# Kernel tuning notes

Hardware: AMD Instinct MI355X
Metric: run time of the kernel (lower is better)

The kernel has to match this reference:

```python
import jax, jax.numpy as jnp
import numpy as np

D = 1024; H = 16; HD = 64; DEPTH = 8; INTERVAL = 4; CTX = 9; NUM_REG = 4
SOFTCAP = 50.0; EPS = 1e-6; ROPE_BASE = 10000.0; IN_DIM = 768; ADIM = 8; FREQ = 256; DH = 4096
B = 1; T = 16; LTOK = 256; S = LTOK + 2 + NUM_REG  # 262 tokens per frame


def setup_inputs() -> dict:
    key = jax.random.key(0)
    ks = jax.random.split(key, 24)
    s = 0.02
    n = jax.random.normal
    inp = {
        'noisy_latents': n(ks[0], (B, T, LTOK, IN_DIM), jnp.float32),
        'signal_levels': jax.random.uniform(ks[1], (B, T), jnp.float32),
        'actions': n(ks[2], (B, T, ADIM), jnp.float32),
        'input_proj_w': n(ks[3], (D, IN_DIM)) * s,
        'noise_w1': n(ks[4], (D, FREQ)) * s,
        'noise_b1': jnp.zeros((D,)),
        'noise_w2': n(ks[5], (D, D)) * s,
        'noise_b2': jnp.zeros((D,)),
        'base_action_embed': n(ks[6], (D,)) * s,
        'action_proj_w': n(ks[7], (D, ADIM)) * (s * 0.1),
        'action_proj_b': jnp.zeros((D,)),
        'register_tokens': n(ks[8], (NUM_REG, D)) * s,
        'ln1_w': jnp.ones((DEPTH, D)),
        's_wqkv': n(ks[9], (DEPTH, 3 * D, D)) * s,
        's_wo': n(ks[10], (DEPTH, D, D)) * s,
        's_qg': jnp.ones((DEPTH, HD)),
        's_kg': jnp.ones((DEPTH, HD)),
        'lnt_w': jnp.ones((DEPTH, D)),
        't_wqkv': n(ks[11], (DEPTH, 3 * D, D)) * s,
        't_wo': n(ks[12], (DEPTH, D, D)) * s,
        't_qg': jnp.ones((DEPTH, HD)),
        't_kg': jnp.ones((DEPTH, HD)),
        'ln2_w': jnp.ones((DEPTH, D)),
        'mlp_w12': n(ks[13], (DEPTH, 2 * DH, D)) * s,
        'mlp_w3': n(ks[14], (DEPTH, D, DH)) * s,
        'final_norm_w': jnp.ones((D,)),
        'out_w': n(ks[15], (IN_DIM, D)) * s,
        'out_b': jnp.zeros((IN_DIM,)),
    }
    return inp


def rms(x, w, eps=EPS):
    return x * jax.lax.rsqrt(jnp.mean(x * x, axis=-1, keepdims=True) + eps) * w


def rope_cache(seq_len):
    inv = ROPE_BASE ** (-jnp.arange(0, HD, 2, dtype=jnp.float32) / HD)  # [HD/2]
    f = jnp.arange(seq_len, dtype=jnp.float32)[:, None] * inv  # [S, HD/2]
    return jnp.cos(f), jnp.sin(f)


def apply_rope(x, cos, sin):
    # x: [..., S, HD]; cos/sin: [S, HD/2]
    x1, x2 = jnp.split(x, 2, axis=-1)
    return jnp.concatenate([x1 * cos - x2 * sin, x1 * sin + x2 * cos], axis=-1)


def attention(xn, wqkv, wo, qg, kg, cos, sin, mask):
    # xn: [B, G, S, D]; mask broadcastable to [..., S, S]
    lead = xn.shape[:-1]
    qkv = jnp.einsum('bgsd,ed->bgse', xn, wqkv)
    q, k, v = jnp.split(qkv, 3, axis=-1)
    def heads(z):
        return z.reshape(lead + (H, HD)).swapaxes(-2, -3)  # [B, G, H, S, HD]
    q, k, v = heads(q), heads(k), heads(v)
    q = rms(q, qg); k = rms(k, kg)  # qk-norm per head
    q = apply_rope(q, cos, sin); k = apply_rope(k, cos, sin)
    logits = jnp.einsum('bghqd,bghkd->bghqk', q, k) / np.sqrt(HD).astype(np.float32)
    logits = SOFTCAP * jnp.tanh(logits / SOFTCAP)  # attn logit softcapping
    logits = jnp.where(mask, logits, -1e30)
    p = jax.nn.softmax(logits, axis=-1)
    o = jnp.einsum('bghqk,bghkd->bghqd', p, v)
    o = o.swapaxes(-2, -3).reshape(lead + (H * HD,))
    return jnp.einsum('bgsd,ed->bgse', o, wo)


def timestep_embedding(t, dim=FREQ, max_period=10000.0):
    half = dim // 2
    freqs = jnp.exp(-np.log(max_period) * jnp.arange(half, dtype=jnp.float32) / half)
    args = t[:, None] * freqs
    return jnp.concatenate([jnp.cos(args), jnp.sin(args)], axis=-1)


def reference(noisy_latents, signal_levels, actions, input_proj_w, noise_w1, noise_b1,
              noise_w2, noise_b2, base_action_embed, action_proj_w, action_proj_b,
              register_tokens, ln1_w, s_wqkv, s_wo, s_qg, s_kg, lnt_w, t_wqkv, t_wo,
              t_qg, t_kg, ln2_w, mlp_w12, mlp_w3, final_norm_w, out_w, out_b):
    b, t, ltok, _ = noisy_latents.shape
    noisy_tokens = jnp.einsum('btld,ed->btle', noisy_latents, input_proj_w)  # [B,T,L,D]
    # timestep embedder (sinusoidal + MLP)
    emb = timestep_embedding(signal_levels.reshape(-1))
    sig = jax.nn.silu(emb @ noise_w1.T + noise_b1) @ noise_w2.T + noise_b2
    sig = sig.reshape(b, t, 1, D)
    act = base_action_embed + actions @ action_proj_w.T + action_proj_b  # [B,T,D]
    act = act[:, :, None, :]
    reg = jnp.broadcast_to(register_tokens, (b, t, NUM_REG, D))
    x = jnp.concatenate([sig, act, reg, noisy_tokens], axis=2)  # [B,T,S,D]
    s = x.shape[2]
    # spatial mask: full attention except frozen token (row 0) attends only to itself
    sm = jnp.ones((s, s), bool)
    sm = sm.at[0].set(False).at[0, 0].set(True)
    # temporal mask: causal with context window CTX
    ti = jnp.arange(t)
    tm = (ti[None, :] <= ti[:, None]) & (ti[None, :] >= ti[:, None] - CTX)
    s_cos, s_sin = rope_cache(s)
    t_cos, t_sin = rope_cache(t)
    for l in range(DEPTH):
        h = rms(x, ln1_w[l])
        x = x + attention(h, s_wqkv[l], s_wo[l], s_qg[l], s_kg[l], s_cos, s_sin, sm)
        if l % INTERVAL == 0:
            xt = x.swapaxes(1, 2)  # [B,S,T,D]
            h = rms(xt, lnt_w[l])
            xt = xt + attention(h, t_wqkv[l], t_wo[l], t_qg[l], t_kg[l], t_cos, t_sin, tm)
            x = xt.swapaxes(1, 2)
        h = rms(x, ln2_w[l])
        g = jnp.einsum('btsd,ed->btse', h, mlp_w12[l])
        g1, g2 = jnp.split(g, 2, axis=-1)
        x = x + jnp.einsum('btse,de->btsd', jax.nn.silu(g1) * g2, mlp_w3[l])
    latents = rms(x[..., NUM_REG + 2:, :], final_norm_w)
    return latents @ out_w.T + out_b  # [B,T,L,IN_DIM]
```

## Files before the change

kernel.cpp:

```cpp
#include <hip/hip_runtime.h>
#include <hip/hip_bf16.h>
#include <math.h>

#define T_ 16
#define S_ 262
#define D_ 1024
#define H_ 16
#define HD_ 64
#define DH_ 4096
#define NTOK (T_*S_)
#define LTOK_ 256
#define INDIM_ 768

typedef __attribute__((ext_vector_type(4))) float f32x4;
typedef __attribute__((ext_vector_type(8))) short s16x8;
typedef __attribute__((ext_vector_type(4))) short s16x4;

__device__ __forceinline__ short f2bf(float f) {
  union { float f; unsigned u; } v; v.f = f;
  unsigned r = v.u + 0x7fffu + ((v.u >> 16) & 1u);
  return (short)(r >> 16);
}
__device__ __forceinline__ float bf2f(short h) {
  union { unsigned u; float f; } v; v.u = ((unsigned)(unsigned short)h) << 16;
  return v.f;
}
__device__ __forceinline__ float softcap(float x) {
  float z = __expf(x * (2.0f / 50.0f));
  return 50.0f * (z - 1.0f) / (z + 1.0f);
}
__device__ __forceinline__ void gload16(const void* g, void* l) {
  __builtin_amdgcn_global_load_lds((const __attribute__((address_space(1))) void*)g,
                                   (__attribute__((address_space(3))) void*)l, 16, 0, 0);
}

template<int SMALL, int RESID, int BIAS, int OUT, int WB, int PERM, int PREP, int ROWMAP>
__global__ __launch_bounds__(256)
void gemm2(const short* __restrict__ A, const void* __restrict__ Wv,
           const float* __restrict__ bias, void* __restrict__ Cv,
           int M, int N, int K,
           const float* __restrict__ qg, const float* __restrict__ kg,
           const float* __restrict__ ctab, const float* __restrict__ stab)
{
  constexpr int BM   = SMALL ? 64 : 128;
  constexpr int MI   = SMALL ? 2 : 4;
  constexpr int WR   = SMALL ? 32 : 64;
  constexpr int NSTG = SMALL ? 2 : 4;
  __shared__ __align__(16) short As[BM*64];
  __shared__ __align__(16) short Bs[BM*64];
  const int tid = threadIdx.x;
  const int m0 = blockIdx.y * BM, n0 = blockIdx.x * BM;
  const int lane = tid & 63, wid = tid >> 6;
  const int wr = (wid >> 1) * WR, wc = (wid & 1) * WR;
  const int lr = lane & 15, lk = (lane >> 4) * 8;
  const short* Wb = (const short*)Wv;
  const float* Wf = (const float*)Wv;

  const f32x4 fzero = {0.f, 0.f, 0.f, 0.f};
  f32x4 acc[MI][MI];
  #pragma unroll
  for (int i = 0; i < MI; ++i)
    #pragma unroll
    for (int j = 0; j < MI; ++j) acc[i][j] = fzero;

  for (int k0 = 0; k0 < K; k0 += 64) {
    #pragma unroll
    for (int i = 0; i < NSTG; ++i) {
      int row = wid*(NSTG*8) + i*8 + (lane >> 3);
      int gm = m0 + row; if (gm >= M) gm = M - 1;
      int gc = (((lane & 7) ^ (row & 7)) << 3);
      gload16(A + (size_t)gm*K + k0 + gc, &As[(wid*(NSTG*8) + i*8)*64]);
    }
    if (WB) {
      #pragma unroll
      for (int i = 0; i < NSTG; ++i) {
        int row = wid*(NSTG*8) + i*8 + (lane >> 3);
        int gc = (((lane & 7) ^ (row & 7)) << 3);
        gload16(Wb + (size_t)(n0 + row)*K + k0 + gc, &Bs[(wid*(NSTG*8) + i*8)*64]);
      }
    } else {
      #pragma unroll
      for (int i = 0; i < NSTG; ++i) {
        int slot = tid + 256*i;
        int row = slot >> 3, c8 = (slot & 7) << 3;
        int gr = n0 + row;
        if (PERM) { int c = gr >> 5, q = gr & 31; gr = (q < 16) ? c*16 + q : DH_ + c*16 + (q - 16); }
        const float* wp = Wf + (size_t)gr*K + k0 + c8;
        float4 w0 = *(const float4*)wp, w1 = *(const float4*)(wp + 4);
        s16x8 b;
        b[0]=f2bf(w0.x); b[1]=f2bf(w0.y); b[2]=f2bf(w0.z); b[3]=f2bf(w0.w);
        b[4]=f2bf(w1.x); b[5]=f2bf(w1.y); b[6]=f2bf(w1.z); b[7]=f2bf(w1.w);
        *(s16x8*)&Bs[row*64 + (c8 ^ ((row & 7) << 3))] = b;
      }
    }
    __syncthreads();
    #pragma unroll
    for (int kh = 0; kh < 2; ++kh) {
      const int col0 = kh*32 + lk;
      s16x8 af[MI], bfr[MI];
      #pragma unroll
      for (int mi = 0; mi < MI; ++mi) {
        int row = wr + mi*16 + lr;
        af[mi] = *(const s16x8*)&As[row*64 + (col0 ^ ((row & 7) << 3))];
      }
      #pragma unroll
      for (int ni = 0; ni < MI; ++ni) {
        int row = wc + ni*16 + lr;
        bfr[ni] = *(const s16x8*)&Bs[row*64 + (col0 ^ ((row & 7) << 3))];
      }
      #pragma unroll
      for (int mi = 0; mi < MI; ++mi)
        #pragma unroll
        for (int ni = 0; ni < MI; ++ni)
          acc[mi][ni] = __builtin_amdgcn_mfma_f32_16x16x32_bf16(af[mi], bfr[ni], acc[mi][ni], 0, 0, 0);
    }
    __syncthreads();
  }
  const int gg = (lane >> 4) * 4;
  if constexpr (OUT == 2) {
    #pragma unroll
    for (int mi = 0; mi < MI; ++mi)
      #pragma unroll
      for (int np = 0; np < MI/2; ++np) {
        const int ni = np*2;
        const int ocol = ((n0 + wc + ni*16) >> 5) * 16 + lr;
        #pragma unroll
        for (int r = 0; r < 4; ++r) {
          int row = m0 + wr + mi*16 + gg + r;
          if (row < M) {
            float g = acc[mi][ni][r], v = acc[mi][ni+1][r];
            float sl = g / (1.f + __expf(-g));
            ((short*)Cv)[(size_t)row * (N >> 1) + ocol] = f2bf(sl * v);
          }
        }
      }
  } else if constexpr (PREP != 0) {
    const int colsec = n0 + wc;
    const bool isv = (colsec >= 2048);
    const float* gp = (colsec < 1024) ? qg : kg;
    float gv[MI];
    if (!isv) {
      #pragma unroll
      for (int ni = 0; ni < MI; ++ni) gv[ni] = gp[ni*16 + lr];
    }
    #pragma unroll
    for (int mi = 0; mi < MI; ++mi) {
      #pragma unroll
      for (int r = 0; r < 4; ++r) {
        int row = m0 + wr + mi*16 + gg + r;
        int rowc = row < M ? row : M - 1;
        float vv[MI];
        #pragma unroll
        for (int ni = 0; ni < MI; ++ni) vv[ni] = acc[mi][ni][r];
        if (!isv) {
          float ss = vv[0]*vv[0] + vv[1]*vv[1] + vv[2]*vv[2] + vv[3]*vv[3];
          ss += __shfl_xor(ss, 1);
          ss += __shfl_xor(ss, 2);
          ss += __shfl_xor(ss, 4);
          ss += __shfl_xor(ss, 8);
          float sc = rsqrtf(ss * (1.f/64.f) + 1e-6f);
          int pos = (PREP == 1) ? (rowc % S_) : (rowc / S_);
          float c0 = ctab[pos*32 + lr],      s0 = stab[pos*32 + lr];
          float c1 = ctab[pos*32 + 16 + lr], s1 = stab[pos*32 + 16 + lr];
          float a0 = vv[0]*sc*gv[0], a1 = vv[1]*sc*gv[1];
          float a2 = vv[2]*sc*gv[2], a3 = vv[3]*sc*gv[3];
          vv[0] = a0*c0 - a2*s0;
          vv[1] = a1*c1 - a3*s1;
          vv[2] = a0*s0 + a2*c0;
          vv[3] = a1*s1 + a3*c1;
        }
        if (row < M) {
          #pragma unroll
          for (int ni = 0; ni < MI; ++ni)
            ((short*)Cv)[(size_t)row * N + n0 + wc + ni*16 + lr] = f2bf(vv[ni]);
        }
      }
    }
  } else {
    #pragma unroll
    for (int mi = 0; mi < MI; ++mi)
      #pragma unroll
      for (int ni = 0; ni < MI; ++ni) {
        int col = n0 + wc + ni*16 + lr;
        #pragma unroll
        for (int r = 0; r < 4; ++r) {
          int row = m0 + wr + mi*16 + gg + r;
          if (row < M) {
            float v = acc[mi][ni][r];
            if (BIAS) v += bias[col];
            size_t orow = ROWMAP ? (size_t)((row >> 8) * S_ + 6 + (row & 255)) : (size_t)row;
            size_t idx = orow * N + col;
            if (RESID == 1)       ((float*)Cv)[idx] += v;
            else if (OUT == 1)    ((short*)Cv)[idx]  = f2bf(v);
            else                  ((float*)Cv)[idx]  = v;
          }
        }
      }
  }
}

template<int FINAL>
__global__ __launch_bounds__(256)
void rmsnorm_k(const float* __restrict__ x, const float* __restrict__ w, short* __restrict__ h)
{
  const int lane = threadIdx.x & 63;
  const int row = blockIdx.x*4 + (threadIdx.x >> 6);
  const int xrow = FINAL ? ((row >> 8) * S_ + 6 + (row & 255)) : row;
  const float* xp = x + (size_t)xrow*D_;
  float4 v[4];
  #pragma unroll
  for (int j = 0; j < 4; ++j) v[j] = *(const float4*)(xp + j*256 + lane*4);
  float ss = 0.f;
  #pragma unroll
  for (int j = 0; j < 4; ++j) ss += v[j].x*v[j].x + v[j].y*v[j].y + v[j].z*v[j].z + v[j].w*v[j].w;
  #pragma unroll
  for (int m = 1; m < 64; m <<= 1) ss += __shfl_xor(ss, m);
  const float sc = rsqrtf(ss * (1.f/1024.f) + 1e-6f);
  #pragma unroll
  for (int j = 0; j < 4; ++j) {
    float4 wv = *(const float4*)(w + j*256 + lane*4);
    s16x4 hv;
    hv[0] = f2bf(v[j].x*sc*wv.x); hv[1] = f2bf(v[j].y*sc*wv.y);
    hv[2] = f2bf(v[j].z*sc*wv.z); hv[3] = f2bf(v[j].w*sc*wv.w);
    *(s16x4*)(h + (size_t)row*D_ + j*256 + lane*4) = hv;
  }
}

__global__ void rope_tab_k(float* __restrict__ ct, float* __restrict__ st, int npos)
{
  int i = blockIdx.x*256 + threadIdx.x;
  if (i >= npos*32) return;
  int pos = i >> 5, fi = i & 31;
  float ang = (float)pos * expf((float)fi * (-9.210340371976184f/32.f));
  float s, c; sincosf(ang, &s, &c);
  ct[i] = c; st[i] = s;
}

__global__ __launch_bounds__(256)
void attn_spatial_k(const short* __restrict__ qkv, short* __restrict__ o)
{
  __shared__ __align__(16) short Vt[64][296];
  __shared__ __align__(16) short Pl[4][16][296];
  const int tid = threadIdx.x;
  const int b = blockIdx.x;
  const int t = b >> 4, h = b & 15;
  const short* kbase = qkv + (size_t)t*S_*3072 + 1024 + h*64;
  const short* vbase = kbase + 1024;
  const s16x8 zv = {0,0,0,0,0,0,0,0};
  #pragma unroll
  for (int i = 0; i < 9; ++i) {
    int slot = tid + 256*i;
    if (slot < 2176) {
      int row = slot >> 3, c8 = (slot & 7) * 8;
      s16x8 v = zv;
      if (row < S_) v = *(const s16x8*)(vbase + (size_t)row*3072 + c8);
      #pragma unroll
      for (int j = 0; j < 8; ++j) Vt[c8 + j][row] = v[j];
    }
  }
  #pragma unroll
  for (int i = 0; i < 6; ++i) {
    int slot = tid + 256*i;
    Vt[slot / 24][272 + (slot % 24)] = 0;
  }
  if (tid < 64) o[(size_t)t*S_*D_ + h*64 + tid] = vbase[tid];
  __syncthreads();

  const int lane = tid & 63, wid = tid >> 6;
  const int lr = lane & 15, lk = (lane >> 4) * 8;
  const int gg = (lane >> 4) * 4;
  const f32x4 fzero = {0.f,0.f,0.f,0.f};

  for (int qt = wid; qt < 17; qt += 4) {
    int qrow = qt*16 + lr; if (qrow >= S_) qrow = 0;
    const short* qbase = qkv + (size_t)(t*S_ + qrow)*3072 + h*64;
    s16x8 qf0 = *(const s16x8*)(qbase + lk);
    s16x8 qf1 = *(const s16x8*)(qbase + 32 + lk);

    f32x4 lg[17];
    #pragma unroll
    for (int nt = 0; nt < 17; ++nt) lg[nt] = fzero;
    __builtin_amdgcn_s_setprio(1);
    #pragma unroll
    for (int nt = 0; nt < 17; ++nt) {
      int krow = nt*16 + lr; if (krow >= S_) krow = S_ - 1;
      s16x8 kf0 = *(const s16x8*)(kbase + (size_t)krow*3072 + lk);
      s16x8 kf1 = *(const s16x8*)(kbase + (size_t)krow*3072 + 32 + lk);
      lg[nt] = __builtin_amdgcn_mfma_f32_16x16x32_bf16(qf0, kf0, lg[nt], 0, 0, 0);
      lg[nt] = __builtin_amdgcn_mfma_f32_16x16x32_bf16(qf1, kf1, lg[nt], 0, 0, 0);
    }
    __builtin_amdgcn_s_setprio(0);
    #pragma unroll
    for (int r = 0; r < 4; ++r) {
      float mx = -1e30f;
      #pragma unroll
      for (int nt = 0; nt < 17; ++nt) {
        float v = softcap(lg[nt][r] * 0.125f);
        if (nt*16 + lr >= S_) v = -1e30f;
        lg[nt][r] = v;
        mx = fmaxf(mx, v);
      }
      mx = fmaxf(mx, __shfl_xor(mx, 1));
      mx = fmaxf(mx, __shfl_xor(mx, 2));
      mx = fmaxf(mx, __shfl_xor(mx, 4));
      mx = fmaxf(mx, __shfl_xor(mx, 8));
      float sum = 0.f;
      #pragma unroll
      for (int nt = 0; nt < 17; ++nt) { float pe = __expf(lg[nt][r] - mx); lg[nt][r] = pe; sum += pe; }
      sum += __shfl_xor(sum, 1);
      sum += __shfl_xor(sum, 2);
      sum += __shfl_xor(sum, 4);
      sum += __shfl_xor(sum, 8);
      float is = 1.f / sum;
      #pragma unroll
      for (int nt = 0; nt < 17; ++nt) Pl[wid][gg + r][nt*16 + lr] = f2bf(lg[nt][r] * is);
      Pl[wid][gg + r][272 + lr] = 0;
    }
    f32x4 oacc[4];
    #pragma unroll
    for (int ni = 0; ni < 4; ++ni) oacc[ni] = fzero;
    __builtin_amdgcn_s_setprio(1);
    #pragma unroll
    for (int ks = 0; ks < 9; ++ks) {
      s16x8 pf = *(const s16x8*)&Pl[wid][lr][ks*32 + lk];
      #pragma unroll
      for (int ni = 0; ni < 4; ++ni) {
        s16x8 vf = *(const s16x8*)&Vt[ni*16 + lr][ks*32 + lk];
        oacc[ni] = __builtin_amdgcn_mfma_f32_16x16x32_bf16(pf, vf, oacc[ni], 0, 0, 0);
      }
    }
    __builtin_amdgcn_s_setprio(0);
    #pragma unroll
    for (int ni = 0; ni < 4; ++ni)
      #pragma unroll
      for (int r = 0; r < 4; ++r) {
        int q = qt*16 + gg + r;
        if (q < S_ && q != 0) o[(size_t)(t*S_ + q)*D_ + h*64 + ni*16 + lr] = f2bf(oacc[ni][r]);
      }
  }
}

__global__ __launch_bounds__(256)
void attn_temporal_k(const short* __restrict__ qkv, short* __restrict__ o)
{
  __shared__ float Ql[4][16][68];
  __shared__ float Kl[4][16][68];
  __shared__ float Vl[4][16][68];
  __shared__ float Pl2[4][16][17];
  const int tid = threadIdx.x, lane = tid & 63, wid = tid >> 6;
  const int gw = blockIdx.x*4 + wid;
  const int s = gw >> 4, h = gw & 15;
  const int tt = lane >> 2, dp = (lane & 3) * 16;
  const short* base = qkv + (size_t)(tt*S_ + s)*3072 + h*64 + dp;
  #pragma unroll
  for (int part = 0; part < 3; ++part) {
    const short* bp = base + part*1024;
    s16x8 v0 = *(const s16x8*)(bp);
    s16x8 v1 = *(const s16x8*)(bp + 8);
    float* dst = (part == 0) ? &Ql[wid][tt][dp] : (part == 1) ? &Kl[wid][tt][dp] : &Vl[wid][tt][dp];
    #pragma unroll
    for (int j = 0; j < 8; ++j) { dst[j] = bf2f(v0[j]); dst[8 + j] = bf2f(v1[j]); }
  }
  __syncthreads();
  const int qr = lane >> 2;
  float qv[64];
  #pragma unroll
  for (int j = 0; j < 64; ++j) qv[j] = Ql[wid][qr][j];
  float pvals[4];
  #pragma unroll
  for (int i = 0; i < 4; ++i) {
    int kt = (lane & 3) + i*4;
    float d = 0.f;
    #pragma unroll
    for (int j = 0; j < 64; ++j) d += qv[j] * Kl[wid][kt][j];
    d *= 0.125f;
    d = softcap(d);
    bool keep = (kt <= qr) && (kt + 9 >= qr);
    pvals[i] = keep ? d : -1e30f;
  }
  float mx = fmaxf(fmaxf(pvals[0], pvals[1]), fmaxf(pvals[2], pvals[3]));
  mx = fmaxf(mx, __shfl_xor(mx, 1));
  mx = fmaxf(mx, __shfl_xor(mx, 2));
  float sum = 0.f;
  #pragma unroll
  for (int i = 0; i < 4; ++i) { pvals[i] = __expf(pvals[i] - mx); sum += pvals[i]; }
  sum += __shfl_xor(sum, 1);
  sum += __shfl_xor(sum, 2);
  float is = 1.f / sum;
  #pragma unroll
  for (int i = 0; i < 4; ++i) Pl2[wid][qr][(lane & 3) + i*4] = pvals[i] * is;
  __syncthreads();
  float acc[16];
  #pragma unroll
  for (int j = 0; j < 16; ++j) acc[j] = 0.f;
  #pragma unroll
  for (int kt = 0; kt < 16; ++kt) {
    float pv = Pl2[wid][qr][kt];
    #pragma unroll
    for (int j = 0; j < 16; ++j) acc[j] += pv * Vl[wid][kt][dp + j];
  }
  short* op = o + (size_t)(qr*S_ + s)*D_ + h*64 + dp;
  #pragma unroll
  for (int j = 0; j < 16; ++j) op[j] = f2bf(acc[j]);
}

struct CvtJobs {
  const float* src[10];
  short* dst[10];
  int end[10];
  int njobs;
};

__global__ void cvt_multi_k(CvtJobs jobs)
{
  int q = blockIdx.x*256 + threadIdx.x;
  int j = 0;
  while (j < jobs.njobs && q >= jobs.end[j]) ++j;
  if (j >= jobs.njobs) return;
  int base = (j == 0) ? 0 : jobs.end[j-1];
  size_t idx = (size_t)(q - base);
  float4 v = *(const float4*)(jobs.src[j] + idx*4);
  s16x4 ov; ov[0]=f2bf(v.x); ov[1]=f2bf(v.y); ov[2]=f2bf(v.z); ov[3]=f2bf(v.w);
  *(s16x4*)(jobs.dst[j] + idx*4) = ov;
}

__global__ void cvt_f32_bf16_k(const float* __restrict__ in, short* __restrict__ out, int n4)
{
  int i = blockIdx.x*256 + threadIdx.x;
  if (i >= n4) return;
  float4 v = *(const float4*)(in + (size_t)i*4);
  s16x4 ov; ov[0]=f2bf(v.x); ov[1]=f2bf(v.y); ov[2]=f2bf(v.z); ov[3]=f2bf(v.w);
  *(s16x4*)(out + (size_t)i*4) = ov;
}

__global__ void cvt_w12_k(const float* __restrict__ in, short* __restrict__ out)
{
  int pb = blockIdx.x;
  int l = pb >> 13, pr = pb & 8191;
  int c = pr >> 5, q = pr & 31;
  int orig = (q < 16) ? c*16 + q : DH_ + c*16 + (q - 16);
  const float* ip = in + ((size_t)l*8192 + orig)*1024 + threadIdx.x*4;
  short* op = out + ((size_t)l*8192 + pr)*1024 + threadIdx.x*4;
  float4 v = *(const float4*)ip;
  s16x4 ov; ov[0]=f2bf(v.x); ov[1]=f2bf(v.y); ov[2]=f2bf(v.z); ov[3]=f2bf(v.w);
  *(s16x4*)op = ov;
}

__global__ void timestep_embed_k(const float* __restrict__ sig, float* __restrict__ emb)
{
  int tid = threadIdx.x;
  int n = tid >> 4;
  int j0 = (tid & 15) * 16;
  float tv = sig[n];
  for (int j = j0; j < j0 + 16; ++j) {
    int half = j & 127;
    float freq = expf(-9.210340371976184f * (float)half / 128.f);
    float a = tv * freq;
    emb[n*256 + j] = (j < 128) ? cosf(a) : sinf(a);
  }
}

__global__ void noise_mlp1_k(const float* __restrict__ emb, const float* __restrict__ w1,
                             const float* __restrict__ b1, float* __restrict__ hid)
{
  const int o = blockIdx.x*256 + threadIdx.x;
  const int n = o >> 10, e = o & 1023;
  const float4* er = (const float4*)(emb + n*256);
  const float4* wr = (const float4*)(w1 + (size_t)e*256);
  float s = b1[e];
  for (int k = 0; k < 64; ++k) { float4 a = er[k]; float4 b = wr[k]; s += a.x*b.x + a.y*b.y + a.z*b.z + a.w*b.w; }
  hid[o] = s / (1.f + __expf(-s));
}

__global__ void noise_mlp2_k(const float* __restrict__ hid, const float* __restrict__ w2,
                             const float* __restrict__ b2, float* __restrict__ sg)
{
  const int o = blockIdx.x*256 + threadIdx.x;
  const int n = o >> 10, e = o & 1023;
  const float4* hr = (const float4*)(hid + n*1024);
  const float4* wr = (const float4*)(w2 + (size_t)e*1024);
  float s = b2[e];
  for (int k = 0; k < 256; ++k) { float4 a = hr[k]; float4 b = wr[k]; s += a.x*b.x + a.y*b.y + a.z*b.z + a.w*b.w; }
  sg[o] = s;
}

__global__ void act_embed_k(const float* __restrict__ actions, const float* __restrict__ base,
                            const float* __restrict__ apw, const float* __restrict__ apb,
                            float* __restrict__ ar)
{
  const int o = blockIdx.x*256 + threadIdx.x;
  const int n = o >> 10, e = o & 1023;
  float s = base[e] + apb[e];
  #pragma unroll
  for (int j = 0; j < 8; ++j) s += actions[n*8 + j] * apw[(size_t)e*8 + j];
  ar[o] = s;
}

__global__ void fill6_k(const float* __restrict__ sig, const float* __restrict__ act,
                        const float* __restrict__ reg, float* __restrict__ x)
{
  const int b = blockIdx.x;
  const int t = b / 6, s = b % 6;
  const int d = threadIdx.x * 4;
  float4 v;
  if (s == 0)      v = *(const float4*)(sig + t*D_ + d);
  else if (s == 1) v = *(const float4*)(act + t*D_ + d);
  else             v = *(const float4*)(reg + (s-2)*D_ + d);
  *(float4*)(x + (size_t)(t*S_ + s)*D_ + d) = v;
}

extern "C" void kernel_launch(void* const* d_in, const int* in_sizes, int n_in,
                              void* d_out, int out_size, void* d_ws, size_t ws_size,
                              hipStream_t stream)
{
  (void)in_sizes; (void)n_in; (void)out_size;
  const float* noisy   = (const float*)d_in[0];
  const float* sig_lv  = (const float*)d_in[1];
  const float* actions = (const float*)d_in[2];
  const float* in_proj = (const float*)d_in[3];
  const float* nw1     = (const float*)d_in[4];
  const float* nb1     = (const float*)d_in[5];
  const float* nw2     = (const float*)d_in[6];
  const float* nb2     = (const float*)d_in[7];
  const float* base_ae = (const float*)d_in[8];
  const float* apw     = (const float*)d_in[9];
  const float* apb     = (const float*)d_in[10];
  const float* regtok  = (const float*)d_in[11];
  const float* ln1w    = (const float*)d_in[12];
  const float* s_wqkv  = (const float*)d_in[13];
  const float* s_wo    = (const float*)d_in[14];
  const float* s_qg    = (const float*)d_in[15];
  const float* s_kg    = (const float*)d_in[16];
  const float* lntw    = (const float*)d_in[17];
  const float* t_wqkv  = (const float*)d_in[18];
  const float* t_wo    = (const float*)d_in[19];
  const float* t_qg    = (const float*)d_in[20];
  const float* t_kg    = (const float*)d_in[21];
  const float* ln2w    = (const float*)d_in[22];
  const float* w12     = (const float*)d_in[23];
  const float* w3      = (const float*)d_in[24];
  const float* fnw     = (const float*)d_in[25];
  const float* outw    = (const float*)d_in[26];
  const float* outb    = (const float*)d_in[27];

  char* p = (char*)d_ws;
  auto take = [&](size_t n) { char* r = p; p += n; return r; };
  float* x   = (float*)take((size_t)NTOK*D_*4);
  short* hb  = (short*)take((size_t)NTOK*D_*2);
  short* qkv = (short*)take((size_t)NTOK*3072*2);
  short* ob  = (short*)take((size_t)NTOK*D_*2);
  short* mb  = qkv;
  short* nlb = (short*)take((size_t)4096*INDIM_*2);
  float* emb = (float*)take(16*256*4);
  float* hid = (float*)take(16*1024*4);
  float* sgb = (float*)take(16*1024*4);
  float* acr = (float*)take(16*1024*4);
  float* csS = (float*)take(S_*32*4);
  float* snS = (float*)take(S_*32*4);
  float* csT = (float*)take(16*32*4);
  float* snT = (float*)take(16*32*4);
  short* wqkv_s_bf = (short*)take((size_t)8*3*D_*D_*2);
  short* wo_s_bf   = (short*)take((size_t)8*D_*D_*2);
  short* wqkv_t_bf = (short*)take((size_t)2*3*D_*D_*2);
  short* wo_t_bf   = (short*)take((size_t)2*D_*D_*2);
  short* w12_bf    = (short*)take((size_t)8*2*DH_*D_*2);
  short* w3_bf     = (short*)take((size_t)8*D_*DH_*2);
  short* inp_bf    = (short*)take((size_t)D_*INDIM_*2);
  short* outw_bf   = (short*)take((size_t)INDIM_*D_*2);
  const size_t full_need = (size_t)(p - (char*)d_ws);
  const bool wb = ws_size >= full_need;

  if (wb) {
    CvtJobs jobs;
    int acc_q = 0, nj = 0;
    auto add = [&](const float* s, short* d, size_t elems) {
      jobs.src[nj] = s; jobs.dst[nj] = d;
      acc_q += (int)(elems / 4); jobs.end[nj] = acc_q; ++nj;
    };
    add(s_wqkv, wqkv_s_bf, (size_t)8*3*D_*D_);
    add(s_wo,   wo_s_bf,   (size_t)8*D_*D_);
    add(t_wqkv,                     wqkv_t_bf,                   (size_t)3*D_*D_);
    add(t_wqkv + (size_t)4*3*D_*D_, wqkv_t_bf + (size_t)3*D_*D_, (size_t)3*D_*D_);
    add(t_wo,                       wo_t_bf,                     (size_t)D_*D_);
    add(t_wo + (size_t)4*D_*D_,     wo_t_bf + (size_t)D_*D_,     (size_t)D_*D_);
    add(w3,   w3_bf,   (size_t)8*D_*DH_);
    add(in_proj, inp_bf, (size_t)D_*INDIM_);
    add(outw,    outw_bf,(size_t)INDIM_*D_);
    add(noisy,   nlb,    (size_t)4096*INDIM_);
    jobs.njobs = nj;
    cvt_multi_k<<<(acc_q + 255)/256, 256, 0, stream>>>(jobs);
    cvt_w12_k<<<65536, 256, 0, stream>>>(w12, w12_bf);
  } else {
    cvt_f32_bf16_k<<<3072, 256, 0, stream>>>(noisy, nlb, 4096*INDIM_/4);
  }
  rope_tab_k<<<33, 256, 0, stream>>>(csS, snS, S_);
  rope_tab_k<<<2,  256, 0, stream>>>(csT, snT, 16);

  timestep_embed_k<<<1, 256, 0, stream>>>(sig_lv, emb);
  noise_mlp1_k<<<64, 256, 0, stream>>>(emb, nw1, nb1, hid);
  noise_mlp2_k<<<64, 256, 0, stream>>>(hid, nw2, nb2, sgb);
  act_embed_k<<<64, 256, 0, stream>>>(actions, base_ae, apw, apb, acr);
  if (wb) gemm2<1,0,0,0,1,0,0,1><<<dim3(16,64), 256, 0, stream>>>(nlb, inp_bf,  nullptr, x, 4096, D_, INDIM_, nullptr, nullptr, nullptr, nullptr);
  else    gemm2<1,0,0,0,0,0,0,1><<<dim3(16,64), 256, 0, stream>>>(nlb, in_proj, nullptr, x, 4096, D_, INDIM_, nullptr, nullptr, nullptr, nullptr);
  fill6_k<<<96, 256, 0, stream>>>(sgb, acr, regtok, x);

  for (int l = 0; l < 8; ++l) {
    rmsnorm_k<0><<<NTOK/4, 256, 0, stream>>>(x, ln1w + l*D_, hb);
    if (wb) gemm2<0,0,0,1,1,0,1,0><<<dim3(24,33), 256, 0, stream>>>(hb, wqkv_s_bf + (size_t)l*3*D_*D_, nullptr, qkv, NTOK, 3*D_, D_, s_qg + l*HD_, s_kg + l*HD_, csS, snS);
    else    gemm2<0,0,0,1,0,0,1,0><<<dim3(24,33), 256, 0, stream>>>(hb, s_wqkv   + (size_t)l*3*D_*D_, nullptr, qkv, NTOK, 3*D_, D_, s_qg + l*HD_, s_kg + l*HD_, csS, snS);
    attn_spatial_k<<<256, 256, 0, stream>>>(qkv, ob);
    if (wb) gemm2<1,1,0,0,1,0,0,0><<<dim3(16,66), 256, 0, stream>>>(ob, wo_s_bf + (size_t)l*D_*D_, nullptr, x, NTOK, D_, D_, nullptr, nullptr, nullptr, nullptr);
    else    gemm2<1,1,0,0,0,0,0,0><<<dim3(16,66), 256, 0, stream>>>(ob, s_wo    + (size_t)l*D_*D_, nullptr, x, NTOK, D_, D_, nullptr, nullptr, nullptr, nullptr);
    if (l % 4 == 0) {
      const int ls = l / 4;
      rmsnorm_k<0><<<NTOK/4, 256, 0, stream>>>(x, lntw + l*D_, hb);
      if (wb) gemm2<0,0,0,1,1,0,2,0><<<dim3(24,33), 256, 0, stream>>>(hb, wqkv_t_bf + (size_t)ls*3*D_*D_, nullptr, qkv, NTOK, 3*D_, D_, t_qg + l*HD_, t_kg + l*HD_, csT, snT);
      else    gemm2<0,0,0,1,0,0,2,0><<<dim3(24,33), 256, 0, stream>>>(hb, t_wqkv    + (size_t)l*3*D_*D_,  nullptr, qkv, NTOK, 3*D_, D_, t_qg + l*HD_, t_kg + l*HD_, csT, snT);
      attn_temporal_k<<<1048, 256, 0, stream>>>(qkv, ob);
      if (wb) gemm2<1,1,0,0,1,0,0,0><<<dim3(16,66), 256, 0, stream>>>(ob, wo_t_bf + (size_t)ls*D_*D_, nullptr, x, NTOK, D_, D_, nullptr, nullptr, nullptr, nullptr);
      else    gemm2<1,1,0,0,0,0,0,0><<<dim3(16,66), 256, 0, stream>>>(ob, t_wo    + (size_t)l*D_*D_,  nullptr, x, NTOK, D_, D_, nullptr, nullptr, nullptr, nullptr);
    }
    rmsnorm_k<0><<<NTOK/4, 256, 0, stream>>>(x, ln2w + l*D_, hb);
    if (wb) gemm2<0,0,0,2,1,0,0,0><<<dim3(64,33), 256, 0, stream>>>(hb, w12_bf + (size_t)l*2*DH_*D_, nullptr, mb, NTOK, 2*DH_, D_, nullptr, nullptr, nullptr, nullptr);
    else    gemm2<0,0,0,2,0,1,0,0><<<dim3(64,33), 256, 0, stream>>>(hb, w12    + (size_t)l*2*DH_*D_, nullptr, mb, NTOK, 2*DH_, D_, nullptr, nullptr, nullptr, nullptr);
    if (wb) gemm2<1,1,0,0,1,0,0,0><<<dim3(16,66), 256, 0, stream>>>(mb, w3_bf + (size_t)l*D_*DH_, nullptr, x, NTOK, D_, DH_, nullptr, nullptr, nullptr, nullptr);
    else    gemm2<1,1,0,0,0,0,0,0><<<dim3(16,66), 256, 0, stream>>>(mb, w3    + (size_t)l*D_*DH_, nullptr, x, NTOK, D_, DH_, nullptr, nullptr, nullptr, nullptr);
  }
  rmsnorm_k<1><<<1024, 256, 0, stream>>>(x, fnw, hb);
  if (wb) gemm2<1,0,1,0,1,0,0,0><<<dim3(12,64), 256, 0, stream>>>(hb, outw_bf, outb, (float*)d_out, 4096, INDIM_, D_, nullptr, nullptr, nullptr, nullptr);
  else    gemm2<1,0,1,0,0,0,0,0><<<dim3(12,64), 256, 0, stream>>>(hb, outw,    outb, (float*)d_out, 4096, INDIM_, D_, nullptr, nullptr, nullptr, nullptr);
}
```

Measured before the change: 2.816 ms.

## Add 256x256-tile 8-wave GEMM kernel with fused SwiGLU for MLP up-projection

Adds a dedicated GEMM kernel for the MLP w12 projection. It uses 256x256 output tiles, 512 threads, a double-buffered direct-to-LDS load pipeline with XOR swizzle, and MFMA 16x16x32 bf16. The SwiGLU activation is fused into the epilogue, relying on the permuted interleaved weight layout. The goal is higher arithmetic intensity and less staging overhead for the largest GEMM. The cost is heavy register pressure from 32 accumulators per thread, 128KB of LDS per block, and a partially wasted last M tile of 4192 rows.

```diff
diff --git a/kernel.cpp b/kernel.cpp
--- a/kernel.cpp
+++ b/kernel.cpp
@@ -32,6 +32,108 @@
 __device__ __forceinline__ void gload16(const void* g, void* l) {
   __builtin_amdgcn_global_load_lds((const __attribute__((address_space(1))) void*)g,
                                    (__attribute__((address_space(3))) void*)l, 16, 0, 0);
+}
+
+__global__ __launch_bounds__(512, 2)
+void gemm256_swiglu(const short* __restrict__ A, const short* __restrict__ W,
+                    short* __restrict__ Cv, int M, int N, int K)
+{
+  __shared__ __align__(16) short lds[2][4][128*64];
+  const int tid = threadIdx.x;
+  const int lane = tid & 63, wid = tid >> 6;
+  const int wm = wid >> 2, wn = wid & 3;
+  const int m0 = blockIdx.y * 256, n0 = blockIdx.x * 256;
+  const int lr = lane & 15, lk = (lane >> 4) * 8;
+  const int gg = (lane >> 4) * 4;
+  const int NKT = K >> 6;
+
+  f32x4 acc[8][4];
+  const f32x4 fzero = {0.f, 0.f, 0.f, 0.f};
+  #pragma unroll
+  for (int i = 0; i < 8; ++i)
+    #pragma unroll
+    for (int j = 0; j < 4; ++j) acc[i][j] = fzero;
+
+  const int selem = (((lane & 7) ^ (lane >> 3)) << 3);
+  auto STAGE = [&](int kt, int buf) {
+    const int k0 = kt << 6;
+    #pragma unroll
+    for (int r = 0; r < 4; ++r) {
+      int grow = m0 + (r >> 1)*128 + (r & 1)*64 + wid*8 + (lane >> 3);
+      if (grow >= M) grow = M - 1;
+      gload16(A + (size_t)grow*K + k0 + selem,
+              &lds[buf][r >> 1][((r & 1)*64 + wid*8)*64]);
+    }
+    #pragma unroll
+    for (int r = 0; r < 4; ++r) {
+      int grow = n0 + (r >> 1)*128 + (r & 1)*64 + wid*8 + (lane >> 3);
+      gload16(W + (size_t)grow*K + k0 + selem,
+              &lds[buf][2 + (r >> 1)][((r & 1)*64 + wid*8)*64]);
+    }
+  };
+
+  s16x8 af[8], bfv[4];
+  auto LDAB = [&](int buf, int kh) {
+    const int cs = (kh*32 + lk) ^ ((lr & 7) << 3);
+    #pragma unroll
+    for (int mi = 0; mi < 8; ++mi)
+      af[mi] = *(const s16x8*)&lds[buf][wm][(mi*16 + lr)*64 + cs];
+    #pragma unroll
+    for (int ni = 0; ni < 4; ++ni)
+      bfv[ni] = *(const s16x8*)&lds[buf][2 + (wn >> 1)][((wn & 1)*64 + ni*16 + lr)*64 + cs];
+  };
+  auto MM = [&]() {
+    __builtin_amdgcn_s_setprio(1);
+    #pragma unroll
+    for (int mi = 0; mi < 8; ++mi)
+      #pragma unroll
+      for (int ni = 0; ni < 4; ++ni)
+        acc[mi][ni] = __builtin_amdgcn_mfma_f32_16x16x32_bf16(af[mi], bfv[ni], acc[mi][ni], 0, 0, 0);
+    __builtin_amdgcn_s_setprio(0);
+  };
+
+  STAGE(0, 0);
+  if (NKT > 1) {
+    STAGE(1, 1);
+    asm volatile("s_waitcnt vmcnt(8)" ::: "memory");
+  } else {
+    asm volatile("s_waitcnt vmcnt(0)" ::: "memory");
+  }
+  __builtin_amdgcn_sched_barrier(0);
+  __builtin_amdgcn_s_barrier();
+
+  for (int kt = 0; kt < NKT; ++kt) {
+    const int cur = kt & 1;
+    LDAB(cur, 0);
+    MM();
+    LDAB(cur, 1);
+    asm volatile("s_waitcnt lgkmcnt(0)" ::: "memory");
+    __builtin_amdgcn_sched_barrier(0);
+    __builtin_amdgcn_s_barrier();
+    if (kt + 2 < NKT) STAGE(kt + 2, cur);
+    MM();
+    if (kt + 2 < NKT) asm volatile("s_waitcnt vmcnt(8)" ::: "memory");
+    else              asm volatile("s_waitcnt vmcnt(0)" ::: "memory");
+    __builtin_amdgcn_sched_barrier(0);
+    __builtin_amdgcn_s_barrier();
+  }
+
+  #pragma unroll
+  for (int mi = 0; mi < 8; ++mi)
+    #pragma unroll
+    for (int np = 0; np < 2; ++np) {
+      const int ni = np * 2;
+      const int ocol = ((n0 + wn*64 + ni*16) >> 5) * 16 + lr;
+      #pragma unroll
+      for (int r = 0; r < 4; ++r) {
+        int row = m0 + wm*128 + mi*16 + gg + r;
+        if (row < M) {
+          float g = acc[mi][ni][r], v = acc[mi][ni+1][r];
+          float sl = g / (1.f + __expf(-g));
+          Cv[(size_t)row * (N >> 1) + ocol] = f2bf(sl * v);
+        }
+      }
+    }
 }
 
 template<int SMALL, int RESID, int BIAS, int OUT, int WB, int PERM, int PREP, int ROWMAP>
@@ -621,8 +723,8 @@
       else    gemm2<1,1,0,0,0,0,0,0><<<dim3(16,66), 256, 0, stream>>>(ob, t_wo    + (size_t)l*D_*D_,  nullptr, x, NTOK, D_, D_, nullptr, nullptr, nullptr, nullptr);
     }
     rmsnorm_k<0><<<NTOK/4, 256, 0, stream>>>(x, ln2w + l*D_, hb);
-    if (wb) gemm2<0,0,0,2,1,0,0,0><<<dim3(64,33), 256, 0, stream>>>(hb, w12_bf + (size_t)l*2*DH_*D_, nullptr, mb, NTOK, 2*DH_, D_, nullptr, nullptr, nullptr, nullptr);
-    else    gemm2<0,0,0,2,0,1,0,0><<<dim3(64,33), 256, 0, stream>>>(hb, w12    + (size_t)l*2*DH_*D_, nullptr, mb, NTOK, 2*DH_, D_, nullptr, nullptr, nullptr, nullptr);
+    if (wb) gemm256_swiglu<<<dim3(32,17), 512, 0, stream>>>(hb, w12_bf + (size_t)l*2*DH_*D_, mb, NTOK, 2*DH_, D_);
+    else    gemm2<0,0,0,2,0,1,0,0><<<dim3(64,33), 256, 0, stream>>>(hb, w12 + (size_t)l*2*DH_*D_, nullptr, mb, NTOK, 2*DH_, D_, nullptr, nullptr, nullptr, nullptr);
     if (wb) gemm2<1,1,0,0,1,0,0,0><<<dim3(16,66), 256, 0, stream>>>(mb, w3_bf + (size_t)l*D_*DH_, nullptr, x, NTOK, D_, DH_, nullptr, nullptr, nullptr, nullptr);
     else    gemm2<1,1,0,0,0,0,0,0><<<dim3(16,66), 256, 0, stream>>>(mb, w3    + (size_t)l*D_*DH_, nullptr, x, NTOK, D_, DH_, nullptr, nullptr, nullptr, nullptr);
   }
```

After: 2.864 ms. Within noise of the previous version (+1.7%).
